# Kernel optimization log

Hardware: AMD Instinct MI355X
Metric: run time of the kernel (lower is better)

The kernel has to match this reference:

```python
import jax, jax.numpy as jnp
import numpy as np

N = 50000          # nodes (num_sensors)
E = 600000         # edges
IN_DIM = 75        # 3 * 25
DIMS = [(75, 128), (128, 128), (128, 32)]  # (in, out) per layer: in->hidden->hidden->bottleneck


def setup_inputs() -> dict:
    key = jax.random.key(0)
    ks = jax.random.split(key, 4 + 5 * len(DIMS))
    inp = {
        "x": jax.random.normal(ks[0], (N, IN_DIM), dtype=jnp.float32),
        "edge_index": jax.random.randint(ks[1], (2, E), 0, N, dtype=jnp.int64),
        "weight": jax.random.uniform(ks[2], (E,), dtype=jnp.float32),
        "sim": jax.random.normal(ks[3], (E, 2), dtype=jnp.float32),
    }
    i = 4
    for l, (cin, cout) in enumerate(DIMS):
        s = jnp.float32(1.0 / np.sqrt(cin))
        inp[f"wr{l}"] = jax.random.normal(ks[i + 0], (cin, cout), dtype=jnp.float32) * s  # real part of complex conv filter
        inp[f"wi{l}"] = jax.random.normal(ks[i + 1], (cin, cout), dtype=jnp.float32) * s  # imag part
        inp[f"cb{l}"] = jnp.zeros((cout,), dtype=jnp.float32)                              # conv bias
        inp[f"lw{l}"] = jax.random.normal(ks[i + 2], (cout, cin), dtype=jnp.float32) * s  # Linear weight (torch layout [out,in])
        inp[f"lb{l}"] = jnp.zeros((cout,), dtype=jnp.float32)                              # Linear bias
        i += 5
    return inp


def _layer(x, src, dst, cr, ci, wr, wi, cb, lw, lb):
    # ModeConvFast: gather source features, scale by complex edge coefficient
    # c = weight * (sim_r + i*sim_i), scatter-add to destination nodes,
    # project with complex filter W = wr + i*wi, keep real part, add bias.
    xs = x[src]                                   # [E, Cin] gather
    agg_r = jax.ops.segment_sum(xs * cr[:, None], dst, num_segments=N)  # [N, Cin]
    agg_i = jax.ops.segment_sum(xs * ci[:, None], dst, num_segments=N)  # [N, Cin]
    conv = agg_r @ wr - agg_i @ wi + cb           # real part of complex matmul
    return jax.nn.relu(conv + x @ lw.T + lb)      # conv(x,...) + lin(x), then relu


def reference(x, edge_index, weight, sim,
              wr0, wi0, cb0, lw0, lb0,
              wr1, wi1, cb1, lw1, lb1,
              wr2, wi2, cb2, lw2, lb2):
    src, dst = edge_index[0], edge_index[1]
    cr = weight * sim[:, 0]                       # [E] real edge coefficient
    ci = weight * sim[:, 1]                       # [E] imag edge coefficient
    layers = [
        (wr0, wi0, cb0, lw0, lb0),
        (wr1, wi1, cb1, lw1, lb1),
        (wr2, wi2, cb2, lw2, lb2),
    ]
    for p in layers:
        x = _layer(x, src, dst, cr, ci, *p)
    return x
```

## Files before the change

kernel.cpp:

```cpp
#include <hip/hip_runtime.h>

#define N_NODES 50000
#define N_EDGES 600000
#define E_PAD_MAX (N_EDGES + N_NODES * 7)

using bf16x8 = __attribute__((ext_vector_type(8))) short;
using f32x4  = __attribute__((ext_vector_type(4))) float;
typedef unsigned int uint32_tt;
typedef unsigned long long u64;

__device__ __forceinline__ unsigned short f2bf(float f) {
    union { float f; unsigned int u; } v; v.f = f;
    unsigned int u = v.u;
    return (unsigned short)((u + 0x7fffu + ((u >> 16) & 1u)) >> 16);
}
__device__ __forceinline__ float bf2f(unsigned int h16) {
    union { unsigned int u; float f; } v; v.u = h16 << 16;
    return v.f;
}

__global__ void prep_kernel(
    const float* __restrict__ x0, unsigned short* __restrict__ xb,
    const float* __restrict__ wr0, const float* __restrict__ wi0,
    const float* __restrict__ lw0, unsigned short* __restrict__ BT0,
    const float* __restrict__ wr1, const float* __restrict__ wi1,
    const float* __restrict__ lw1, unsigned short* __restrict__ BT1,
    const float* __restrict__ wr2, const float* __restrict__ wi2,
    const float* __restrict__ lw2, unsigned short* __restrict__ BT2,
    int* __restrict__ cnt, uint2* __restrict__ edat, int n) {
    int tid = blockIdx.x * 256 + threadIdx.x;
    int nth = gridDim.x * 256;
    for (int i = tid; i < N_NODES; i += nth) cnt[i] = 0;
    uint2 z; z.x = 0u; z.y = 0u;
    for (int i = tid; i < E_PAD_MAX; i += nth) edat[i] = z;

    int i = tid;
    int nconv = n * 96;
    if (i < nconv) {
        int r = i / 96, c = i - r * 96;
        xb[i] = (c < 75) ? f2bf(x0[r * 75 + c]) : (unsigned short)0;
        return;
    }
    i -= nconv;
    if (i < 128 * 288) {
        int nn = i / 288, k = i - nn * 288;
        int part = k / 96, kk = k - part * 96;
        float v = 0.f;
        if (kk < 75) {
            if (part == 0)      v = wr0[kk * 128 + nn];
            else if (part == 1) v = -wi0[kk * 128 + nn];
            else                v = lw0[nn * 75 + kk];
        }
        BT0[i] = f2bf(v);
        return;
    }
    i -= 128 * 288;
    if (i < 128 * 384) {
        int nn = i / 384, k = i - nn * 384;
        int part = k >> 7, kk = k & 127;
        float v;
        if (part == 0)      v = wr1[kk * 128 + nn];
        else if (part == 1) v = -wi1[kk * 128 + nn];
        else                v = lw1[nn * 128 + kk];
        BT1[i] = f2bf(v);
        return;
    }
    i -= 128 * 384;
    if (i < 96 * 128) {
        int nn = i >> 7, k = i & 127;
        float v;
        if (nn < 32)      v = wr2[k * 32 + nn];
        else if (nn < 64) v = -wi2[k * 32 + (nn - 32)];
        else              v = lw2[(nn - 64) * 128 + k];
        BT2[i] = f2bf(v);
    }
}


__global__ void hist_kernel(const int* __restrict__ ei, int* __restrict__ cnt,
                            int* __restrict__ rank, int E) {
    int e = blockIdx.x * 256 + threadIdx.x;
    if (e < E) rank[e] = atomicAdd(&cnt[ei[E + e]], 1);
}

__global__ void scan1(const int* __restrict__ deg, int* __restrict__ out,
                      int* __restrict__ bsum, int n) {
    __shared__ int s[256];
    int t = threadIdx.x;
    int base = blockIdx.x * 1024 + t * 4;
    int v0 = (base + 0 < n) ? ((deg[base + 0] + 7) & ~7) : 0;
    int v1 = (base + 1 < n) ? ((deg[base + 1] + 7) & ~7) : 0;
    int v2 = (base + 2 < n) ? ((deg[base + 2] + 7) & ~7) : 0;
    int v3 = (base + 3 < n) ? ((deg[base + 3] + 7) & ~7) : 0;
    int tsum = v0 + v1 + v2 + v3;
    s[t] = tsum;
    __syncthreads();
    for (int off = 1; off < 256; off <<= 1) {
        int tmp = (t >= off) ? s[t - off] : 0;
        __syncthreads();
        s[t] += tmp;
        __syncthreads();
    }
    int excl = s[t] - tsum;
    if (base + 0 < n) out[base + 0] = excl;
    if (base + 1 < n) out[base + 1] = excl + v0;
    if (base + 2 < n) out[base + 2] = excl + v0 + v1;
    if (base + 3 < n) out[base + 3] = excl + v0 + v1 + v2;
    if (t == 255) bsum[blockIdx.x] = s[255];
}

__global__ void scan3(int* __restrict__ off, const int* __restrict__ bsum,
                      int n, int nb) {
    __shared__ int sp;
    int b = blockIdx.x, t = threadIdx.x;
    int seg = b >> 2;
    if (t == 0) {
        int acc = 0;
        for (int k = 0; k < seg; ++k) acc += bsum[k];
        sp = acc;
    }
    __syncthreads();
    int i = b * 256 + t;
    if (i < n) off[i] += sp;
    if (i == n) {
        int tot = sp;
        for (int k = seg; k < nb; ++k) tot += bsum[k];
        off[n] = tot;
    }
}

__global__ void scatter_kernel(const int* __restrict__ ei, const float* __restrict__ w,
                               const float* __restrict__ sim, const int* __restrict__ off,
                               const int* __restrict__ rank, uint2* __restrict__ edat,
                               int E) {
    int e = blockIdx.x * 256 + threadIdx.x;
    if (e >= E) return;
    int s = ei[e], d = ei[E + e];
    int p = off[d] + rank[e];
    float wt = w[e];
    uint2 m;
    m.x = (unsigned)s;
    m.y = (uint32_tt)f2bf(wt * sim[2 * e]) |
          ((uint32_tt)f2bf(wt * sim[2 * e + 1]) << 16);
    edat[p] = m;
}

template <int CU2>
__global__ __launch_bounds__(256) void agg_pair(
    const uint32_tt* __restrict__ x, const int* __restrict__ off,
    const uint2* __restrict__ edat, uint32_tt* __restrict__ aggR,
    uint32_tt* __restrict__ aggI, int n) {
    constexpr int P = CU2 / 2;
    constexpr int RB = CU2 * 4;
    int wave = threadIdx.x >> 6;
    int lane = threadIdx.x & 63;
    int node = __builtin_amdgcn_readfirstlane(blockIdx.x * 4 + wave);
    if (node >= n) return;
    int j = lane >> 5;
    int c = lane & 31;
    int lc = (P == 32) ? c : (c < P ? c : P - 1);
    float ar0 = 0.f, ar1 = 0.f, ar2 = 0.f, ar3 = 0.f;
    float ai0 = 0.f, ai1 = 0.f, ai2 = 0.f, ai3 = 0.f;
    int e0 = __builtin_amdgcn_readfirstlane(off[node]);
    int e1 = __builtin_amdgcn_readfirstlane(off[node + 1]);

    if (e0 < e1) {
        uint2 mn[8];
        int soc[4]; float crc[4], cic[4];
        uint2 wc[4];
        {
            uint2 m0[8];
#pragma unroll
            for (int k = 0; k < 8; ++k) m0[k] = edat[e0 + k];
            int so8[8]; float cr8[8], ci8[8];
#pragma unroll
            for (int k = 0; k < 8; ++k) {
                int s = __builtin_amdgcn_readfirstlane((int)m0[k].x);
                int pk = __builtin_amdgcn_readfirstlane((int)m0[k].y);
                so8[k] = s * RB;
                cr8[k] = bf2f((unsigned)pk & 0xffffu);
                ci8[k] = bf2f((unsigned)pk >> 16);
            }
#pragma unroll
            for (int k = 0; k < 4; ++k) {
                soc[k] = j ? so8[2 * k + 1] : so8[2 * k];
                crc[k] = j ? cr8[2 * k + 1] : cr8[2 * k];
                cic[k] = j ? ci8[2 * k + 1] : ci8[2 * k];
            }
            int nb = (e0 + 8 < e1) ? e0 + 8 : e0;
#pragma unroll
            for (int k = 0; k < 8; ++k) mn[k] = edat[nb + k];
#pragma unroll
            for (int k = 0; k < 4; ++k)
                wc[k] = *(const uint2*)((const char*)x + (unsigned)soc[k] +
                                        (unsigned)(lc * 8));
        }
        for (int e = e0;; e += 8) {
            bool more = (e + 8 < e1);
            int son[4]; float crn[4], cin_[4]; uint2 wn[4];
            if (more) {
                int so8[8]; float cr8[8], ci8[8];
#pragma unroll
                for (int k = 0; k < 8; ++k) {
                    int s = __builtin_amdgcn_readfirstlane((int)mn[k].x);
                    int pk = __builtin_amdgcn_readfirstlane((int)mn[k].y);
                    so8[k] = s * RB;
                    cr8[k] = bf2f((unsigned)pk & 0xffffu);
                    ci8[k] = bf2f((unsigned)pk >> 16);
                }
#pragma unroll
                for (int k = 0; k < 4; ++k) {
                    son[k] = j ? so8[2 * k + 1] : so8[2 * k];
                    crn[k] = j ? cr8[2 * k + 1] : cr8[2 * k];
                    cin_[k] = j ? ci8[2 * k + 1] : ci8[2 * k];
                }
                int nb = (e + 16 < e1) ? e + 16 : e + 8;
#pragma unroll
                for (int k = 0; k < 8; ++k) mn[k] = edat[nb + k];
#pragma unroll
                for (int k = 0; k < 4; ++k)
                    wn[k] = *(const uint2*)((const char*)x + (unsigned)son[k] +
                                            (unsigned)(lc * 8));
            }
#pragma unroll
            for (int k = 0; k < 4; ++k) {
                float lo0 = bf2f(wc[k].x & 0xffffu), hi0 = bf2f(wc[k].x >> 16);
                float lo1 = bf2f(wc[k].y & 0xffffu), hi1 = bf2f(wc[k].y >> 16);
                ar0 += crc[k] * lo0; ar1 += crc[k] * hi0;
                ar2 += crc[k] * lo1; ar3 += crc[k] * hi1;
                ai0 += cic[k] * lo0; ai1 += cic[k] * hi0;
                ai2 += cic[k] * lo1; ai3 += cic[k] * hi1;
            }
            if (!more) break;
#pragma unroll
            for (int k = 0; k < 4; ++k) {
                crc[k] = crn[k]; cic[k] = cin_[k]; wc[k] = wn[k];
            }
        }
    }
    ar0 += __shfl_xor(ar0, 32); ar1 += __shfl_xor(ar1, 32);
    ar2 += __shfl_xor(ar2, 32); ar3 += __shfl_xor(ar3, 32);
    ai0 += __shfl_xor(ai0, 32); ai1 += __shfl_xor(ai1, 32);
    ai2 += __shfl_xor(ai2, 32); ai3 += __shfl_xor(ai3, 32);
    if (lane < P) {
        uint2 oR, oI;
        oR.x = (uint32_tt)f2bf(ar0) | ((uint32_tt)f2bf(ar1) << 16);
        oR.y = (uint32_tt)f2bf(ar2) | ((uint32_tt)f2bf(ar3) << 16);
        oI.x = (uint32_tt)f2bf(ai0) | ((uint32_tt)f2bf(ai1) << 16);
        oI.y = (uint32_tt)f2bf(ai2) | ((uint32_tt)f2bf(ai3) << 16);
        ((uint2*)(aggR + (size_t)node * CU2))[lane] = oR;
        ((uint2*)(aggI + (size_t)node * CU2))[lane] = oI;
    }
}

__global__ __launch_bounds__(256) void agg_out(
    const uint32_tt* __restrict__ Y, const int* __restrict__ off,
    const uint2* __restrict__ edat, const float* __restrict__ cb,
    const float* __restrict__ lb, float* __restrict__ out, int n) {
    int wave = threadIdx.x >> 6;
    int lane = threadIdx.x & 63;
    int node = __builtin_amdgcn_readfirstlane(blockIdx.x * 4 + wave);
    if (node >= n) return;
    int j = lane >> 5;
    int lc = lane & 31;
    int usei = lc >> 4;
    float alo = 0.f, ahi = 0.f;
    int e0 = __builtin_amdgcn_readfirstlane(off[node]);
    int e1 = __builtin_amdgcn_readfirstlane(off[node + 1]);

    if (e0 < e1) {
        uint2 mn[8];
        int soc[4]; float cc[4]; uint32_tt wc[4];
        {
            uint2 m0[8];
#pragma unroll
            for (int k = 0; k < 8; ++k) m0[k] = edat[e0 + k];
            int so8[8]; float cr8[8], ci8[8];
#pragma unroll
            for (int k = 0; k < 8; ++k) {
                int s = __builtin_amdgcn_readfirstlane((int)m0[k].x);
                int pk = __builtin_amdgcn_readfirstlane((int)m0[k].y);
                so8[k] = s * 192;
                cr8[k] = bf2f((unsigned)pk & 0xffffu);
                ci8[k] = bf2f((unsigned)pk >> 16);
            }
#pragma unroll
            for (int k = 0; k < 4; ++k) {
                soc[k] = j ? so8[2 * k + 1] : so8[2 * k];
                float a = j ? cr8[2 * k + 1] : cr8[2 * k];
                float b = j ? ci8[2 * k + 1] : ci8[2 * k];
                cc[k] = usei ? b : a;
            }
            int nb = (e0 + 8 < e1) ? e0 + 8 : e0;
#pragma unroll
            for (int k = 0; k < 8; ++k) mn[k] = edat[nb + k];
#pragma unroll
            for (int k = 0; k < 4; ++k)
                wc[k] = *(const uint32_tt*)((const char*)Y + (unsigned)soc[k] +
                                            (unsigned)(lc * 4));
        }
        for (int e = e0;; e += 8) {
            bool more = (e + 8 < e1);
            int son[4]; float cn[4]; uint32_tt wn[4];
            if (more) {
                int so8[8]; float cr8[8], ci8[8];
#pragma unroll
                for (int k = 0; k < 8; ++k) {
                    int s = __builtin_amdgcn_readfirstlane((int)mn[k].x);
                    int pk = __builtin_amdgcn_readfirstlane((int)mn[k].y);
                    so8[k] = s * 192;
                    cr8[k] = bf2f((unsigned)pk & 0xffffu);
                    ci8[k] = bf2f((unsigned)pk >> 16);
                }
#pragma unroll
                for (int k = 0; k < 4; ++k) {
                    son[k] = j ? so8[2 * k + 1] : so8[2 * k];
                    float a = j ? cr8[2 * k + 1] : cr8[2 * k];
                    float b = j ? ci8[2 * k + 1] : ci8[2 * k];
                    cn[k] = usei ? b : a;
                }
                int nb = (e + 16 < e1) ? e + 16 : e + 8;
#pragma unroll
                for (int k = 0; k < 8; ++k) mn[k] = edat[nb + k];
#pragma unroll
                for (int k = 0; k < 4; ++k)
                    wn[k] = *(const uint32_tt*)((const char*)Y + (unsigned)son[k] +
                                                (unsigned)(lc * 4));
            }
#pragma unroll
            for (int k = 0; k < 4; ++k) {
                float lo = bf2f(wc[k] & 0xffffu), hi = bf2f(wc[k] >> 16);
                alo += cc[k] * lo; ahi += cc[k] * hi;
            }
            if (!more) break;
#pragma unroll
            for (int k = 0; k < 4; ++k) { cc[k] = cn[k]; wc[k] = wn[k]; }
        }
    }
    alo += __shfl_xor(alo, 32); alo += __shfl_xor(alo, 16);
    ahi += __shfl_xor(ahi, 32); ahi += __shfl_xor(ahi, 16);
    if (lane < 16) {
        uint32_tt lin = Y[(size_t)node * 48 + 32 + lane];
        int c0 = 2 * lane, c1 = 2 * lane + 1;
        float v0 = alo + bf2f(lin & 0xffffu) + cb[c0] + lb[c0];
        float v1 = ahi + bf2f(lin >> 16) + cb[c1] + lb[c1];
        float2 r;
        r.x = v0 > 0.f ? v0 : 0.f;
        r.y = v1 > 0.f ? v1 : 0.f;
        ((float2*)out)[(size_t)node * 16 + lane] = r;
    }
}

template <int CINP, int COUT, int BM, int WM, int WN, int MT, int NT,
          bool OUT_BF16, bool RAW, int PARTS>
__global__ __launch_bounds__(256) void gemm_mfma(
    const unsigned short* __restrict__ A0, const unsigned short* __restrict__ A1,
    const unsigned short* __restrict__ A2, const unsigned short* __restrict__ BT,
    const float* __restrict__ cb, const float* __restrict__ lb,
    void* __restrict__ outv, int n) {
    constexpr int PK = 40;
    constexpr int KTOT = PARTS * CINP;
    constexpr int NCH = KTOT / 32;
    constexpr int CPP = CINP / 32;
    __shared__ unsigned short sA[BM][PK];
    __shared__ unsigned short sB[COUT][PK];

    int t = threadIdx.x;
    int lane = t & 63, wave = t >> 6;
    int wm = wave / WN, wn = wave % WN;
    int ml = lane & 15, kh = lane >> 4;
    int node0 = blockIdx.x * BM;

    const unsigned short* Asrc[3] = {A0, A1, A2};

    f32x4 acc[MT][NT];
#pragma unroll
    for (int mt = 0; mt < MT; ++mt)
#pragma unroll
        for (int nt = 0; nt < NT; ++nt) acc[mt][nt] = (f32x4){0.f, 0.f, 0.f, 0.f};

    for (int c = 0; c < NCH; ++c) {
        int part = (PARTS == 1) ? 0 : (c / CPP);
        int kk = (c - part * CPP) * 32;
        const unsigned short* __restrict__ Ap = Asrc[part];
        __syncthreads();
#pragma unroll
        for (int i = t; i < BM * 4; i += 256) {
            int r = i >> 2, q = i & 3;
            int node = node0 + r;
            if (node >= n) node = n - 1;
            *(uint4*)&sA[r][q * 8] =
                *(const uint4*)(Ap + (size_t)node * CINP + kk + q * 8);
        }
#pragma unroll
        for (int i = t; i < COUT * 4; i += 256) {
            int r = i >> 2, q = i & 3;
            *(uint4*)&sB[r][q * 8] =
                *(const uint4*)(BT + (size_t)r * KTOT + c * 32 + q * 8);
        }
        __syncthreads();
        bf16x8 af[MT], bfr[NT];
#pragma unroll
        for (int mt = 0; mt < MT; ++mt)
            af[mt] = *(const bf16x8*)&sA[wm * (MT * 16) + mt * 16 + ml][kh * 8];
#pragma unroll
        for (int nt = 0; nt < NT; ++nt)
            bfr[nt] = *(const bf16x8*)&sB[wn * (NT * 16) + nt * 16 + ml][kh * 8];
#pragma unroll
        for (int mt = 0; mt < MT; ++mt)
#pragma unroll
            for (int nt = 0; nt < NT; ++nt)
                acc[mt][nt] = __builtin_amdgcn_mfma_f32_16x16x32_bf16(
                    af[mt], bfr[nt], acc[mt][nt], 0, 0, 0);
    }

    int row0 = kh * 4;
#pragma unroll
    for (int nt = 0; nt < NT; ++nt) {
        int col = wn * (NT * 16) + nt * 16 + ml;
        float bias = RAW ? 0.f : (cb[col] + lb[col]);
#pragma unroll
        for (int mt = 0; mt < MT; ++mt) {
#pragma unroll
            for (int r = 0; r < 4; ++r) {
                int node = node0 + wm * (MT * 16) + mt * 16 + row0 + r;
                if (node < n) {
                    float v = acc[mt][nt][r] + bias;
                    if (!RAW) v = v > 0.f ? v : 0.f;
                    if (OUT_BF16)
                        ((unsigned short*)outv)[(size_t)node * COUT + col] = f2bf(v);
                    else
                        ((float*)outv)[(size_t)node * COUT + col] = v;
                }
            }
        }
    }
}

__global__ __launch_bounds__(256) void gemm_l1y(
    const unsigned short* __restrict__ A0, const unsigned short* __restrict__ A1,
    const unsigned short* __restrict__ A2, const unsigned short* __restrict__ BT,
    const unsigned short* __restrict__ BT2, const float* __restrict__ cb,
    const float* __restrict__ lb, unsigned short* __restrict__ Yout, int n) {
    constexpr int PK = 40;
    constexpr int PH = 136;
    __shared__ unsigned short sA[128][PK];
    __shared__ unsigned short sB[128][PK];
    __shared__ unsigned short sH[128][PH];

    int t = threadIdx.x;
    int lane = t & 63, wave = t >> 6;
    int wm = wave >> 1, wn = wave & 1;
    int ml = lane & 15, kh = lane >> 4;
    int node0 = blockIdx.x * 128;
    const unsigned short* Asrc[3] = {A0, A1, A2};

    f32x4 acc[4][4];
#pragma unroll
    for (int mt = 0; mt < 4; ++mt)
#pragma unroll
        for (int nt = 0; nt < 4; ++nt) acc[mt][nt] = (f32x4){0.f, 0.f, 0.f, 0.f};

    for (int c = 0; c < 12; ++c) {
        int part = c >> 2;
        int kk = (c & 3) * 32;
        const unsigned short* __restrict__ Ap = Asrc[part];
        __syncthreads();
#pragma unroll
        for (int i = t; i < 512; i += 256) {
            int r = i >> 2, q = i & 3;
            int node = node0 + r;
            if (node >= n) node = n - 1;
            *(uint4*)&sA[r][q * 8] =
                *(const uint4*)(Ap + (size_t)node * 128 + kk + q * 8);
        }
#pragma unroll
        for (int i = t; i < 512; i += 256) {
            int r = i >> 2, q = i & 3;
            *(uint4*)&sB[r][q * 8] =
                *(const uint4*)(BT + (size_t)r * 384 + c * 32 + q * 8);
        }
        __syncthreads();
        bf16x8 af[4], bfr[4];
#pragma unroll
        for (int mt = 0; mt < 4; ++mt)
            af[mt] = *(const bf16x8*)&sA[wm * 64 + mt * 16 + ml][kh * 8];
#pragma unroll
        for (int nt = 0; nt < 4; ++nt)
            bfr[nt] = *(const bf16x8*)&sB[wn * 64 + nt * 16 + ml][kh * 8];
#pragma unroll
        for (int mt = 0; mt < 4; ++mt)
#pragma unroll
            for (int nt = 0; nt < 4; ++nt)
                acc[mt][nt] = __builtin_amdgcn_mfma_f32_16x16x32_bf16(
                    af[mt], bfr[nt], acc[mt][nt], 0, 0, 0);
    }

    int row0 = kh * 4;
#pragma unroll
    for (int nt = 0; nt < 4; ++nt) {
        int col = wn * 64 + nt * 16 + ml;
        float bias = cb[col] + lb[col];
#pragma unroll
        for (int mt = 0; mt < 4; ++mt) {
#pragma unroll
            for (int r = 0; r < 4; ++r) {
                int nl = wm * 64 + mt * 16 + row0 + r;
                float v = acc[mt][nt][r] + bias;
                sH[nl][col] = f2bf(v > 0.f ? v : 0.f);
            }
        }
    }
    __syncthreads();

    f32x4 acc2[4][3];
#pragma unroll
    for (int mt = 0; mt < 4; ++mt)
#pragma unroll
        for (int nt = 0; nt < 3; ++nt) acc2[mt][nt] = (f32x4){0.f, 0.f, 0.f, 0.f};
    for (int c2 = 0; c2 < 4; ++c2) {
        bf16x8 af[4], bfr[3];
#pragma unroll
        for (int mt = 0; mt < 4; ++mt)
            af[mt] = *(const bf16x8*)&sH[wm * 64 + mt * 16 + ml][c2 * 32 + kh * 8];
#pragma unroll
        for (int nt = 0; nt < 3; ++nt) {
            int ycol = wn * 48 + nt * 16 + ml;
            bfr[nt] = *(const bf16x8*)(BT2 + (size_t)ycol * 128 + c2 * 32 + kh * 8);
        }
#pragma unroll
        for (int mt = 0; mt < 4; ++mt)
#pragma unroll
            for (int nt = 0; nt < 3; ++nt)
                acc2[mt][nt] = __builtin_amdgcn_mfma_f32_16x16x32_bf16(
                    af[mt], bfr[nt], acc2[mt][nt], 0, 0, 0);
    }
#pragma unroll
    for (int nt = 0; nt < 3; ++nt) {
        int ycol = wn * 48 + nt * 16 + ml;
#pragma unroll
        for (int mt = 0; mt < 4; ++mt) {
#pragma unroll
            for (int r = 0; r < 4; ++r) {
                int node = node0 + wm * 64 + mt * 16 + row0 + r;
                if (node < n)
                    Yout[(size_t)node * 96 + ycol] = f2bf(acc2[mt][nt][r]);
            }
        }
    }
}


extern "C" void kernel_launch(void* const* d_in, const int* in_sizes, int n_in,
                              void* d_out, int out_size, void* d_ws, size_t ws_size,
                              hipStream_t stream) {
    const float* x0  = (const float*)d_in[0];
    const int*   ei  = (const int*)d_in[1];
    const float* wgt = (const float*)d_in[2];
    const float* sim = (const float*)d_in[3];
    const float *wr[3], *wi[3], *cb[3], *lw[3], *lb[3];
    for (int l = 0; l < 3; ++l) {
        wr[l] = (const float*)d_in[4 + 5 * l];
        wi[l] = (const float*)d_in[5 + 5 * l];
        cb[l] = (const float*)d_in[6 + 5 * l];
        lw[l] = (const float*)d_in[7 + 5 * l];
        lb[l] = (const float*)d_in[8 + 5 * l];
    }

    char* p = (char*)d_ws;
    auto alloc = [&](size_t bytes) -> void* {
        void* r = p;
        p += (bytes + 255) & ~(size_t)255;
        return r;
    };
    int*   off  = (int*)alloc((N_NODES + 1) * 4);
    int*   cnt  = (int*)alloc(N_NODES * 4);
    int*   bsum = (int*)alloc(256);
    int*   rank = (int*)alloc((size_t)N_EDGES * 4);
    uint2* edat = (uint2*)alloc((size_t)E_PAD_MAX * 8);
    unsigned short* xb    = (unsigned short*)alloc((size_t)N_NODES * 96 * 2);
    unsigned short* aggRb = (unsigned short*)alloc((size_t)N_NODES * 128 * 2);
    unsigned short* aggIb = (unsigned short*)alloc((size_t)N_NODES * 128 * 2);
    unsigned short* h1b   = (unsigned short*)alloc((size_t)N_NODES * 128 * 2);
    unsigned short* Yb    = (unsigned short*)alloc((size_t)N_NODES * 96 * 2);
    unsigned short* BT0   = (unsigned short*)alloc((size_t)128 * 288 * 2);
    unsigned short* BT1   = (unsigned short*)alloc((size_t)128 * 384 * 2);
    unsigned short* BT2   = (unsigned short*)alloc((size_t)96 * 128 * 2);
    float* outp = (float*)d_out;

    {
        int total = N_NODES * 96 + 128 * 288 + 128 * 384 + 96 * 128;
        prep_kernel<<<(total + 255) / 256, 256, 0, stream>>>(
            x0, xb, wr[0], wi[0], lw[0], BT0, wr[1], wi[1], lw[1], BT1,
            wr[2], wi[2], lw[2], BT2, cnt, edat, N_NODES);
    }
    hist_kernel<<<(N_EDGES + 255) / 256, 256, 0, stream>>>(ei, cnt, rank, N_EDGES);
    int nb = (N_NODES + 1023) / 1024;
    scan1<<<nb, 256, 0, stream>>>(cnt, off, bsum, N_NODES);
    scan3<<<(N_NODES + 1 + 255) / 256, 256, 0, stream>>>(off, bsum, N_NODES, nb);
    scatter_kernel<<<(N_EDGES + 255) / 256, 256, 0, stream>>>(ei, wgt, sim, off, rank,
                                                              edat, N_EDGES);

    int agrid = (N_NODES + 3) / 4;

    agg_pair<48><<<agrid, 256, 0, stream>>>((const uint32_tt*)xb, off, edat,
                                            (uint32_tt*)aggRb, (uint32_tt*)aggIb, N_NODES);
    gemm_mfma<96, 128, 128, 2, 2, 4, 4, true, false, 3>
        <<<(N_NODES + 127) / 128, 256, 0, stream>>>(aggRb, aggIb, xb, BT0, cb[0], lb[0],
                                                    h1b, N_NODES);
    agg_pair<64><<<agrid, 256, 0, stream>>>((const uint32_tt*)h1b, off, edat,
                                            (uint32_tt*)aggRb, (uint32_tt*)aggIb, N_NODES);
    gemm_l1y<<<(N_NODES + 127) / 128, 256, 0, stream>>>(aggRb, aggIb, h1b, BT1, BT2,
                                                        cb[1], lb[1], Yb, N_NODES);
    agg_out<<<agrid, 256, 0, stream>>>((const uint32_tt*)Yb, off, edat, cb[2], lb[2],
                                       outp, N_NODES);
}
```

Before: 257.3 us.

## Fuse CSR build into one cooperative kernel and use packed FMA in aggregation

```diff
diff --git a/kernel.cpp b/kernel.cpp
--- a/kernel.cpp
+++ b/kernel.cpp
@@ -1,4 +1,7 @@
 #include <hip/hip_runtime.h>
+#include <hip/hip_cooperative_groups.h>
+
+namespace cg = cooperative_groups;
 
 #define N_NODES 50000
 #define N_EDGES 600000
@@ -6,6 +9,7 @@
 
 using bf16x8 = __attribute__((ext_vector_type(8))) short;
 using f32x4  = __attribute__((ext_vector_type(4))) float;
+using f32x2  = __attribute__((ext_vector_type(2))) float;
 typedef unsigned int uint32_tt;
 typedef unsigned long long u64;
 
@@ -17,6 +21,11 @@
 __device__ __forceinline__ float bf2f(unsigned int h16) {
     union { unsigned int u; float f; } v; v.u = h16 << 16;
     return v.f;
+}
+__device__ __forceinline__ f32x2 unpk(uint32_tt w) {
+    union { uint32_tt u; float f; } a, b;
+    a.u = w << 16; b.u = w & 0xffff0000u;
+    return (f32x2){a.f, b.f};
 }
 
 __global__ void prep_kernel(
@@ -76,73 +85,60 @@
     }
 }
 
-
-__global__ void hist_kernel(const int* __restrict__ ei, int* __restrict__ cnt,
-                            int* __restrict__ rank, int E) {
-    int e = blockIdx.x * 256 + threadIdx.x;
-    if (e < E) rank[e] = atomicAdd(&cnt[ei[E + e]], 1);
-}
-
-__global__ void scan1(const int* __restrict__ deg, int* __restrict__ out,
-                      int* __restrict__ bsum, int n) {
+__global__ __launch_bounds__(256) void graph_build(
+    const int* __restrict__ ei, const float* __restrict__ w,
+    const float* __restrict__ sim, int* __restrict__ cnt,
+    int* __restrict__ rank, int* __restrict__ off,
+    int* __restrict__ bscan, uint2* __restrict__ edat, int n, int E) {
+    cg::grid_group grid = cg::this_grid();
+    int t = threadIdx.x, b = blockIdx.x;
+    int tid = b * 256 + t;
+    int nth = gridDim.x * 256;
+
+    for (int e = tid; e < E; e += nth)
+        rank[e] = atomicAdd(&cnt[ei[E + e]], 1);
+    grid.sync();
+
     __shared__ int s[256];
-    int t = threadIdx.x;
-    int base = blockIdx.x * 1024 + t * 4;
-    int v0 = (base + 0 < n) ? ((deg[base + 0] + 7) & ~7) : 0;
-    int v1 = (base + 1 < n) ? ((deg[base + 1] + 7) & ~7) : 0;
-    int v2 = (base + 2 < n) ? ((deg[base + 2] + 7) & ~7) : 0;
-    int v3 = (base + 3 < n) ? ((deg[base + 3] + 7) & ~7) : 0;
-    int tsum = v0 + v1 + v2 + v3;
-    s[t] = tsum;
+    int i = tid;
+    int deg = (i < n) ? ((cnt[i] + 7) & ~7) : 0;
+    s[t] = deg;
     __syncthreads();
-    for (int off = 1; off < 256; off <<= 1) {
-        int tmp = (t >= off) ? s[t - off] : 0;
+    for (int o = 1; o < 256; o <<= 1) {
+        int tmp = (t >= o) ? s[t - o] : 0;
         __syncthreads();
         s[t] += tmp;
         __syncthreads();
     }
-    int excl = s[t] - tsum;
-    if (base + 0 < n) out[base + 0] = excl;
-    if (base + 1 < n) out[base + 1] = excl + v0;
-    if (base + 2 < n) out[base + 2] = excl + v0 + v1;
-    if (base + 3 < n) out[base + 3] = excl + v0 + v1 + v2;
-    if (t == 255) bsum[blockIdx.x] = s[255];
-}
-
-__global__ void scan3(int* __restrict__ off, const int* __restrict__ bsum,
-                      int n, int nb) {
-    __shared__ int sp;
-    int b = blockIdx.x, t = threadIdx.x;
-    int seg = b >> 2;
-    if (t == 0) {
-        int acc = 0;
-        for (int k = 0; k < seg; ++k) acc += bsum[k];
-        sp = acc;
-    }
-    __syncthreads();
-    int i = b * 256 + t;
-    if (i < n) off[i] += sp;
-    if (i == n) {
-        int tot = sp;
-        for (int k = seg; k < nb; ++k) tot += bsum[k];
-        off[n] = tot;
-    }
-}
-
-__global__ void scatter_kernel(const int* __restrict__ ei, const float* __restrict__ w,
-                               const float* __restrict__ sim, const int* __restrict__ off,
-                               const int* __restrict__ rank, uint2* __restrict__ edat,
-                               int E) {
-    int e = blockIdx.x * 256 + threadIdx.x;
-    if (e >= E) return;
-    int s = ei[e], d = ei[E + e];
-    int p = off[d] + rank[e];
-    float wt = w[e];
-    uint2 m;
-    m.x = (unsigned)s;
-    m.y = (uint32_tt)f2bf(wt * sim[2 * e]) |
-          ((uint32_tt)f2bf(wt * sim[2 * e + 1]) << 16);
-    edat[p] = m;
+    int incl = s[t];
+    if (t == 255) bscan[b] = incl;
+    grid.sync();
+    if (b == 0) {
+        int v = bscan[t];
+        s[t] = v;
+        __syncthreads();
+        for (int o = 1; o < 256; o <<= 1) {
+            int tmp = (t >= o) ? s[t - o] : 0;
+            __syncthreads();
+            s[t] += tmp;
+            __syncthreads();
+        }
+        bscan[t] = s[t] - v;
+    }
+    grid.sync();
+    if (i <= n) off[i] = bscan[b] + incl - deg;
+    grid.sync();
+
+    for (int e = tid; e < E; e += nth) {
+        int sid = ei[e], d = ei[E + e];
+        int pos = off[d] + rank[e];
+        float wt = w[e];
+        uint2 m;
+        m.x = (unsigned)sid;
+        m.y = (uint32_tt)f2bf(wt * sim[2 * e]) |
+              ((uint32_tt)f2bf(wt * sim[2 * e + 1]) << 16);
+        edat[pos] = m;
+    }
 }
 
 template <int CU2>
@@ -159,8 +155,8 @@
     int j = lane >> 5;
     int c = lane & 31;
     int lc = (P == 32) ? c : (c < P ? c : P - 1);
-    float ar0 = 0.f, ar1 = 0.f, ar2 = 0.f, ar3 = 0.f;
-    float ai0 = 0.f, ai1 = 0.f, ai2 = 0.f, ai3 = 0.f;
+    f32x2 arA = (f32x2){0.f, 0.f}, arB = (f32x2){0.f, 0.f};
+    f32x2 aiA = (f32x2){0.f, 0.f}, aiB = (f32x2){0.f, 0.f};
     int e0 = __builtin_amdgcn_readfirstlane(off[node]);
     int e1 = __builtin_amdgcn_readfirstlane(off[node + 1]);
 
@@ -224,12 +220,14 @@
             }
 #pragma unroll
             for (int k = 0; k < 4; ++k) {
-                float lo0 = bf2f(wc[k].x & 0xffffu), hi0 = bf2f(wc[k].x >> 16);
-                float lo1 = bf2f(wc[k].y & 0xffffu), hi1 = bf2f(wc[k].y >> 16);
-                ar0 += crc[k] * lo0; ar1 += crc[k] * hi0;
-                ar2 += crc[k] * lo1; ar3 += crc[k] * hi1;
-                ai0 += cic[k] * lo0; ai1 += cic[k] * hi0;
-                ai2 += cic[k] * lo1; ai3 += cic[k] * hi1;
+                f32x2 w0 = unpk(wc[k].x);
+                f32x2 w1 = unpk(wc[k].y);
+                f32x2 cr2 = (f32x2){crc[k], crc[k]};
+                f32x2 ci2 = (f32x2){cic[k], cic[k]};
+                arA = cr2 * w0 + arA;
+                arB = cr2 * w1 + arB;
+                aiA = ci2 * w0 + aiA;
+                aiB = ci2 * w1 + aiB;
             }
             if (!more) break;
 #pragma unroll
@@ -238,6 +236,8 @@
             }
         }
     }
+    float ar0 = arA.x, ar1 = arA.y, ar2 = arB.x, ar3 = arB.y;
+    float ai0 = aiA.x, ai1 = aiA.y, ai2 = aiB.x, ai3 = aiB.y;
     ar0 += __shfl_xor(ar0, 32); ar1 += __shfl_xor(ar1, 32);
     ar2 += __shfl_xor(ar2, 32); ar3 += __shfl_xor(ar3, 32);
     ai0 += __shfl_xor(ai0, 32); ai1 += __shfl_xor(ai1, 32);
@@ -264,7 +264,7 @@
     int j = lane >> 5;
     int lc = lane & 31;
     int usei = lc >> 4;
-    float alo = 0.f, ahi = 0.f;
+    f32x2 acc = (f32x2){0.f, 0.f};
     int e0 = __builtin_amdgcn_readfirstlane(off[node]);
     int e1 = __builtin_amdgcn_readfirstlane(off[node + 1]);
 
@@ -329,14 +329,16 @@
             }
 #pragma unroll
             for (int k = 0; k < 4; ++k) {
-                float lo = bf2f(wc[k] & 0xffffu), hi = bf2f(wc[k] >> 16);
-                alo += cc[k] * lo; ahi += cc[k] * hi;
+                f32x2 wv = unpk(wc[k]);
+                f32x2 c2 = (f32x2){cc[k], cc[k]};
+                acc = c2 * wv + acc;
             }
             if (!more) break;
 #pragma unroll
             for (int k = 0; k < 4; ++k) { cc[k] = cn[k]; wc[k] = wn[k]; }
         }
     }
+    float alo = acc.x, ahi = acc.y;
     alo += __shfl_xor(alo, 32); alo += __shfl_xor(alo, 16);
     ahi += __shfl_xor(ahi, 32); ahi += __shfl_xor(ahi, 16);
     if (lane < 16) {
@@ -575,7 +577,7 @@
     };
     int*   off  = (int*)alloc((N_NODES + 1) * 4);
     int*   cnt  = (int*)alloc(N_NODES * 4);
-    int*   bsum = (int*)alloc(256);
+    int*   bscan = (int*)alloc(256 * 4);
     int*   rank = (int*)alloc((size_t)N_EDGES * 4);
     uint2* edat = (uint2*)alloc((size_t)E_PAD_MAX * 8);
     unsigned short* xb    = (unsigned short*)alloc((size_t)N_NODES * 96 * 2);
@@ -594,12 +596,14 @@
             x0, xb, wr[0], wi[0], lw[0], BT0, wr[1], wi[1], lw[1], BT1,
             wr[2], wi[2], lw[2], BT2, cnt, edat, N_NODES);
     }
-    hist_kernel<<<(N_EDGES + 255) / 256, 256, 0, stream>>>(ei, cnt, rank, N_EDGES);
-    int nb = (N_NODES + 1023) / 1024;
-    scan1<<<nb, 256, 0, stream>>>(cnt, off, bsum, N_NODES);
-    scan3<<<(N_NODES + 1 + 255) / 256, 256, 0, stream>>>(off, bsum, N_NODES, nb);
-    scatter_kernel<<<(N_EDGES + 255) / 256, 256, 0, stream>>>(ei, wgt, sim, off, rank,
-                                                              edat, N_EDGES);
+    {
+        int nN = N_NODES, nE = N_EDGES;
+        void* args[] = {(void*)&ei, (void*)&wgt, (void*)&sim, (void*)&cnt,
+                        (void*)&rank, (void*)&off, (void*)&bscan, (void*)&edat,
+                        (void*)&nN, (void*)&nE};
+        hipLaunchCooperativeKernel((const void*)graph_build, dim3(256), dim3(256),
+                                   args, 0, stream);
+    }
 
     int agrid = (N_NODES + 3) / 4;
 
```

New measurement: 404.0 us. 1.57x slower.
